# Kernel tuning notes

Hardware: AMD Instinct MI355X
Metric: run time of the kernel (lower is better)

Reference implementation:

```python
import jax, jax.numpy as jnp
import numpy as np

B, N, D, K = 2, 8192, 512, 16


def setup_inputs() -> dict:
    key = jax.random.key(0)
    k1, k2, k3, k4 = jax.random.split(key, 4)
    x = jax.random.normal(k1, (B, N, D), dtype=jnp.float32)
    xyz = jax.random.normal(k2, (B, N, 3), dtype=jnp.float32)
    # nn.Linear(d_model, 3*d_model): weight [3D, D], bias [3D]
    W_qkv = jax.random.normal(k3, (3 * D, D), dtype=jnp.float32) * 0.02
    b_qkv = jnp.zeros((3 * D,), dtype=jnp.float32)
    # nn.Linear(d_model, d_model)
    W_fc = jax.random.normal(k4, (D, D), dtype=jnp.float32) * 0.02
    b_fc = jnp.zeros((D,), dtype=jnp.float32)
    return {"x": x, "xyz": xyz, "W_qkv": W_qkv, "b_qkv": b_qkv, "W_fc": W_fc, "b_fc": b_fc}


def _knn_idx(xyz):
    # squared-distance KNN (same ordering as cdist): |a|^2 + |b|^2 - 2 a.b
    sq = jnp.sum(xyz * xyz, axis=-1)                      # [B, N]
    d2 = sq[:, :, None] + sq[:, None, :] - 2.0 * jnp.einsum('bnc,bmc->bnm', xyz, xyz)
    return jax.lax.top_k(-d2, K)[1]                       # [B, N, K] smallest distances


def reference(x, xyz, W_qkv, b_qkv, W_fc, b_fc):
    knn_idx = _knn_idx(xyz)                               # no-grad in original
    qkv = jnp.einsum('bnd,ed->bne', x, W_qkv) + b_qkv     # [B, N, 3D]
    qkv = qkv.reshape(B, N, 3, D)
    q, k, v = qkv[:, :, 0], qkv[:, :, 1], qkv[:, :, 2]    # [B, N, D]
    gather = jax.vmap(lambda arr, idx: arr[idx])          # per-batch neighbor gather
    k_neigh = gather(k, knn_idx)                          # [B, N, K, D]
    v_neigh = gather(v, knn_idx)                          # [B, N, K, D]
    # faithful to einsum('bnd,bnsk->bns', q, k_neigh): sums d and feature dims independently
    attn = (q.sum(-1)[:, :, None] * k_neigh.sum(-1)) / jnp.sqrt(jnp.float32(D))  # [B, N, K]
    attn = jax.nn.softmax(attn, axis=2)[..., None]        # [B, N, K, 1]
    x_out = (attn * v_neigh).sum(axis=2)                  # [B, N, D]
    return jnp.einsum('bnd,ed->bne', x_out, W_fc) + b_fc + x
```

## Files before the change

kernel.cpp:

```cpp
#include <hip/hip_runtime.h>

typedef _Float16 half_t;
typedef _Float16 half8 __attribute__((ext_vector_type(8)));
typedef _Float16 half4v __attribute__((ext_vector_type(4)));
typedef float f32x4 __attribute__((ext_vector_type(4)));
typedef float f32x2 __attribute__((ext_vector_type(2)));

#define NB 2
#define NN 8192
#define ND 512
#define NKNN 16
#define BN (NB*NN)

#define OFF_XH   0ull
#define OFF_VH   (OFF_XH  + (size_t)BN*ND*2)
#define OFF_XOH  (OFF_VH  + (size_t)BN*ND*2)
#define OFF_WVH  (OFF_XOH + (size_t)BN*ND*2)
#define OFF_WFCH (OFF_WVH + (size_t)ND*ND*2)
#define OFF_XW   (OFF_WFCH+ (size_t)ND*ND*2)
#define OFF_XW2  (OFF_XW  + (size_t)BN*16)
#define OFF_IDX  (OFF_XW2 + (size_t)BN*16)
#define OFF_WQC  (OFF_IDX + (size_t)BN*NKNN*4)
#define OFF_WKC  (OFF_WQC + 2048)
#define OFF_QKB  (OFF_WKC + 2048)
#define OFF_QS   (OFF_QKB + 256)
#define OFF_KS   (OFF_QS  + (size_t)BN*4)

__device__ __forceinline__ void gload16(const void* g, void* l) {
  __builtin_amdgcn_global_load_lds((const __attribute__((address_space(1))) void*)g,
                                   (__attribute__((address_space(3))) void*)l, 16, 0, 0);
}

__global__ __launch_bounds__(256) void ksetup(const float* __restrict__ wqkv,
                                              const float* __restrict__ bqkv,
                                              const float* __restrict__ wfc,
                                              const float* __restrict__ xyz,
                                              float* __restrict__ wq, float* __restrict__ wk,
                                              float* __restrict__ qkb,
                                              half_t* __restrict__ wvh, half_t* __restrict__ wfch,
                                              float4* __restrict__ xw, float4* __restrict__ xw2) {
  const int blk = blockIdx.x;
  const int t = threadIdx.x;
  if (blk < 16) {
    int h = blk >> 3, g = blk & 7;
    int dl = t & 63, s = t >> 6;
    const float* Wb = wqkv + (size_t)h * 512 * 512;
    int d = g * 64 + dl;
    float acc = 0.f;
    for (int e = s * 128; e < s * 128 + 128; ++e) acc += Wb[(size_t)e * 512 + d];
    __shared__ float red[4][64];
    red[s][dl] = acc;
    __syncthreads();
    if (s == 0) (h ? wk : wq)[d] = red[0][dl] + red[1][dl] + red[2][dl] + red[3][dl];
  } else if (blk == 16) {
    __shared__ float r0[256], r1[256];
    r0[t] = bqkv[t] + bqkv[t + 256];
    r1[t] = bqkv[512 + t] + bqkv[768 + t];
    __syncthreads();
    for (int s = 128; s; s >>= 1) {
      if (t < s) { r0[t] += r0[t + s]; r1[t] += r1[t + s]; }
      __syncthreads();
    }
    if (t == 0) { qkb[0] = r0[0]; qkb[1] = r1[0]; }
  } else if (blk < 273) {
    int i = (blk - 17) * 256 + t;
    float4 a = ((const float4*)(wqkv + 1024 * 512))[i];
    half4v ha; ha[0]=(half_t)a.x; ha[1]=(half_t)a.y; ha[2]=(half_t)a.z; ha[3]=(half_t)a.w;
    *(half4v*)(wvh + (size_t)i * 4) = ha;
    float4 c = ((const float4*)wfc)[i];
    half4v hc; hc[0]=(half_t)c.x; hc[1]=(half_t)c.y; hc[2]=(half_t)c.z; hc[3]=(half_t)c.w;
    *(half4v*)(wfch + (size_t)i * 4) = hc;
  } else {
    int p = (blk - 273) * 256 + t;
    int b = p >> 12;
    int pl = p & 4095;
    int i0 = b * NN + pl * 2;
    const float* s = xyz + (size_t)i0 * 3;
    float x0 = s[0], y0 = s[1], z0 = s[2];
    float x1 = s[3], y1 = s[4], z1 = s[5];
    float sq0 = __fadd_rn(__fadd_rn(__fmul_rn(x0, x0), __fmul_rn(y0, y0)), __fmul_rn(z0, z0));
    float sq1 = __fadd_rn(__fadd_rn(__fmul_rn(x1, x1), __fmul_rn(y1, y1)), __fmul_rn(z1, z1));
    xw[i0]     = make_float4(x0, y0, z0, sq0);
    xw[i0 + 1] = make_float4(x1, y1, z1, sq1);
    xw2[(size_t)b * NN + pl]        = make_float4(x0, x1, y0, y1);
    xw2[(size_t)b * NN + NN/2 + pl] = make_float4(z0, z1, sq0, sq1);
  }
}

__global__ __launch_bounds__(256) void kxh(const float* __restrict__ x,
                                           const float* __restrict__ wq,
                                           const float* __restrict__ wk,
                                           const float* __restrict__ qkb,
                                           half_t* __restrict__ xh,
                                           float* __restrict__ qs,
                                           float* __restrict__ ks) {
  int wid = blockIdx.x * 4 + (threadIdx.x >> 6);
  int l = threadIdx.x & 63;
  size_t base = (size_t)wid * ND + l * 8;
  float4 a0 = *(const float4*)(x + base);
  float4 a1 = *(const float4*)(x + base + 4);
  half8 h;
  h[0]=(half_t)a0.x; h[1]=(half_t)a0.y; h[2]=(half_t)a0.z; h[3]=(half_t)a0.w;
  h[4]=(half_t)a1.x; h[5]=(half_t)a1.y; h[6]=(half_t)a1.z; h[7]=(half_t)a1.w;
  *(half8*)(xh + base) = h;
  float4 q0 = ((const float4*)(wq + l * 8))[0], q1 = ((const float4*)(wq + l * 8))[1];
  float4 k0 = ((const float4*)(wk + l * 8))[0], k1 = ((const float4*)(wk + l * 8))[1];
  float dq = a0.x*q0.x + a0.y*q0.y + a0.z*q0.z + a0.w*q0.w
           + a1.x*q1.x + a1.y*q1.y + a1.z*q1.z + a1.w*q1.w;
  float dk = a0.x*k0.x + a0.y*k0.y + a0.z*k0.z + a0.w*k0.w
           + a1.x*k1.x + a1.y*k1.y + a1.z*k1.z + a1.w*k1.w;
  #pragma unroll
  for (int o = 32; o; o >>= 1) { dq += __shfl_xor(dq, o); dk += __shfl_xor(dk, o); }
  if (l == 0) { qs[wid] = dq + qkb[0]; ks[wid] = dk + qkb[1]; }
}

#define QPW 4
#define KTILE 256
__global__ __launch_bounds__(256, 6) void kknn(const float4* __restrict__ xw,
                                               const float4* __restrict__ xw2,
                                               int* __restrict__ idxo) {
  __shared__ __align__(16) float4 ldsA[2][KTILE];
  __shared__ __align__(16) float4 ldsB[2][KTILE];
  __shared__ float qdl[16 * 64];
  __shared__ int   qil[16 * 64];
  const int tid = threadIdx.x;
  const int l = tid & 63;
  const int w = tid >> 6;
  const int b = blockIdx.x >> 9;
  const int qbase = (blockIdx.x & 511) * (4 * QPW) + w * QPW;
  const float4* xb  = xw  + (size_t)b * NN;
  const float4* xa2 = xw2 + (size_t)b * NN;
  const float4* xb2 = xa2 + NN / 2;

#define STAGE(t, bi) do {                                                        \
    int ts_ = (t) * KTILE;                                                       \
    gload16(xa2 + ts_ + w * 64 + l, (void*)&ldsA[bi][w * 64]);                   \
    gload16(xb2 + ts_ + w * 64 + l, (void*)&ldsB[bi][w * 64]);                   \
  } while (0)

  f32x2 qxx[QPW], qyy[QPW], qzz[QPW], qww[QPW];
  #pragma unroll
  for (int qi = 0; qi < QPW; ++qi) {
    float4 qp = xb[qbase + qi];
    qxx[qi] = (f32x2){qp.x, qp.x};
    qyy[qi] = (f32x2){qp.y, qp.y};
    qzz[qi] = (f32x2){qp.z, qp.z};
    qww[qi] = (f32x2){qp.w, qp.w};
  }
  const f32x2 m2 = (f32x2){-2.0f, -2.0f};

  #pragma unroll
  for (int qi = 0; qi < QPW; ++qi) {
    qdl[(w * 4 + qi) * 64 + l] = __builtin_inff();
    qil[(w * 4 + qi) * 64 + l] = 0x7fffffff;
  }

  f32x2 mind[QPW];
  #pragma unroll
  for (int qi = 0; qi < QPW; ++qi) mind[qi] = (f32x2){__builtin_inff(), __builtin_inff()};

  STAGE(0, 0);
  __syncthreads();
  for (int t = 0; t < 16; ++t) {
    if (t < 15) STAGE(t + 1, (t + 1) & 1);
    #pragma unroll
    for (int it = 0; it < 4; ++it) {
      int p = it * 64 + l;
      float4 A  = ldsA[t & 1][p];
      float4 Bv = ldsB[t & 1][p];
      f32x2 cx = (f32x2){A.x, A.y};
      f32x2 cy = (f32x2){A.z, A.w};
      f32x2 cz = (f32x2){Bv.x, Bv.y};
      f32x2 cw = (f32x2){Bv.z, Bv.w};
      #pragma unroll
      for (int qi = 0; qi < QPW; ++qi) {
        f32x2 dot = __builtin_elementwise_fma(qzz[qi], cz,
                      __builtin_elementwise_fma(qyy[qi], cy, qxx[qi] * cx));
        f32x2 s2 = qww[qi] + cw;
        f32x2 d2 = __builtin_elementwise_fma(m2, dot, s2);
        mind[qi] = __builtin_elementwise_min(mind[qi], d2);
      }
    }
    __syncthreads();
  }

  float wst[QPW];
  #pragma unroll
  for (int qi = 0; qi < QPW; ++qi) {
    float d = fminf(mind[qi][0], mind[qi][1]);
    #pragma unroll
    for (int k = 2; k <= 64; k <<= 1) {
      #pragma unroll
      for (int j = k >> 1; j > 0; j >>= 1) {
        float od = __shfl_xor(d, j);
        bool up = ((l & k) == 0);
        bool lower_lane = ((l & j) == 0);
        bool oless = od < d;
        bool take = (up == lower_lane) ? oless : !oless;
        if (take) d = od;
      }
    }
    wst[qi] = __shfl(d, 15);
  }

  int qcnt[QPW];
  #pragma unroll
  for (int qi = 0; qi < QPW; ++qi) qcnt[qi] = 0;
  const unsigned long long below = (1ull << l) - 1;

  __syncthreads();
  STAGE(0, 0);
  __syncthreads();
  for (int t = 0; t < 16; ++t) {
    if (t < 15) STAGE(t + 1, (t + 1) & 1);
    #pragma unroll 2
    for (int it = 0; it < 4; ++it) {
      int p = it * 64 + l;
      float4 A  = ldsA[t & 1][p];
      float4 Bv = ldsB[t & 1][p];
      f32x2 cx = (f32x2){A.x, A.y};
      f32x2 cy = (f32x2){A.z, A.w};
      f32x2 cz = (f32x2){Bv.x, Bv.y};
      f32x2 cw = (f32x2){Bv.z, Bv.w};
      int ci0 = (t * KTILE + p) * 2;
      #pragma unroll
      for (int qi = 0; qi < QPW; ++qi) {
        f32x2 dot = __builtin_elementwise_fma(qzz[qi], cz,
                      __builtin_elementwise_fma(qyy[qi], cy, qxx[qi] * cx));
        f32x2 s2 = qww[qi] + cw;
        f32x2 d2 = __builtin_elementwise_fma(m2, dot, s2);
        bool ok0 = d2[0] <= wst[qi];
        bool ok1 = d2[1] <= wst[qi];
        unsigned long long m0 = __ballot(ok0);
        if (m0) {
          int slot = qcnt[qi] + __popcll(m0 & below);
          if (ok0 && slot < 64) {
            qdl[(w * 4 + qi) * 64 + slot] = d2[0];
            qil[(w * 4 + qi) * 64 + slot] = ci0;
          }
          qcnt[qi] += __popcll(m0);
        }
        unsigned long long m1 = __ballot(ok1);
        if (m1) {
          int slot = qcnt[qi] + __popcll(m1 & below);
          if (ok1 && slot < 64) {
            qdl[(w * 4 + qi) * 64 + slot] = d2[1];
            qil[(w * 4 + qi) * 64 + slot] = ci0 + 1;
          }
          qcnt[qi] += __popcll(m1);
        }
      }
    }
    __syncthreads();
  }

  #pragma unroll
  for (int qi = 0; qi < QPW; ++qi) {
    float d = qdl[(w * 4 + qi) * 64 + l];
    int  ii = qil[(w * 4 + qi) * 64 + l];
    #pragma unroll
    for (int k = 2; k <= 64; k <<= 1) {
      #pragma unroll
      for (int j = k >> 1; j > 0; j >>= 1) {
        float od = __shfl_xor(d, j);
        int   oi = __shfl_xor(ii, j);
        bool up = ((l & k) == 0);
        bool lower_lane = ((l & j) == 0);
        bool oless = (od < d) || (od == d && oi < ii);
        bool take = (up == lower_lane) ? oless : !oless;
        if (take) { d = od; ii = oi; }
      }
    }
    if (l < 16) idxo[((size_t)b * NN + qbase + qi) * NKNN + l] = ii;
  }
#undef STAGE
}

template <int EPI>
__global__ __launch_bounds__(256) void kgemm(const half_t* __restrict__ A,
                                             const half_t* __restrict__ Bw,
                                             const float* __restrict__ bias,
                                             const float* __restrict__ resid,
                                             void* __restrict__ Cout) {
  __shared__ __align__(16) half_t As[128 * 64];
  __shared__ __align__(16) half_t Bs[128 * 64];
  const int tid = threadIdx.x;
  const int l = tid & 63;
  const int w = tid >> 6;
  const int wm = w >> 1, wn = w & 1;
  const int mt = blockIdx.x >> 2;
  const int nt = blockIdx.x & 3;
  const int lr = l & 15, lg = l >> 4;

  f32x4 acc[4][4];
  #pragma unroll
  for (int i = 0; i < 4; ++i)
    #pragma unroll
    for (int j = 0; j < 4; ++j) acc[i][j] = (f32x4){0.f, 0.f, 0.f, 0.f};

  for (int kt = 0; kt < 8; ++kt) {
    #pragma unroll
    for (int i = 0; i < 4; ++i) {
      int id = i * 256 + tid;
      int rr = id >> 3, cc = id & 7;
      gload16(A + (size_t)(mt * 128 + rr) * ND + kt * 64 + cc * 8,
              (void*)(As + (size_t)(i * 256 + w * 64) * 8));
      gload16(Bw + (size_t)(nt * 128 + rr) * ND + kt * 64 + cc * 8,
              (void*)(Bs + (size_t)(i * 256 + w * 64) * 8));
    }
    __syncthreads();
    #pragma unroll
    for (int kk = 0; kk < 2; ++kk) {
      half8 af[4], bf[4];
      #pragma unroll
      for (int mi = 0; mi < 4; ++mi)
        af[mi] = *(const half8*)(As + (wm * 64 + mi * 16 + lr) * 64 + kk * 32 + lg * 8);
      #pragma unroll
      for (int ni = 0; ni < 4; ++ni)
        bf[ni] = *(const half8*)(Bs + (wn * 64 + ni * 16 + lr) * 64 + kk * 32 + lg * 8);
      #pragma unroll
      for (int mi = 0; mi < 4; ++mi)
        #pragma unroll
        for (int ni = 0; ni < 4; ++ni)
          acc[mi][ni] = __builtin_amdgcn_mfma_f32_16x16x32_f16(af[mi], bf[ni], acc[mi][ni], 0, 0, 0);
    }
    __syncthreads();
  }

  #pragma unroll
  for (int mi = 0; mi < 4; ++mi) {
    #pragma unroll
    for (int ni = 0; ni < 4; ++ni) {
      int col = nt * 128 + wn * 64 + ni * 16 + lr;
      #pragma unroll
      for (int r4 = 0; r4 < 4; ++r4) {
        size_t row = (size_t)mt * 128 + wm * 64 + mi * 16 + lg * 4 + r4;
        float v = acc[mi][ni][r4] + bias[col];
        if (EPI == 0) ((half_t*)Cout)[row * ND + col] = (half_t)v;
        else          ((float*)Cout)[row * ND + col] = v + resid[row * ND + col];
      }
    }
  }
}

__global__ __launch_bounds__(256) void kattn(const int* __restrict__ idx,
                                             const float* __restrict__ qs,
                                             const float* __restrict__ ks,
                                             const half_t* __restrict__ vh,
                                             half_t* __restrict__ xoh) {
  int wid = blockIdx.x * 4 + (threadIdx.x >> 6);
  int l = threadIdx.x & 63;
  int b = wid >> 13;
  int j = l & 15;
  int nb = idx[(size_t)wid * NKNN + j];
  float ksv = ks[(size_t)b * NN + nb];
  float logit = __fdiv_rn(__fmul_rn(qs[wid], ksv), 22.627416997969522f);
  float mx = logit;
  #pragma unroll
  for (int o = 8; o; o >>= 1) mx = fmaxf(mx, __shfl_xor(mx, o, 16));
  float e = expf(logit - mx);
  float s = e;
  #pragma unroll
  for (int o = 8; o; o >>= 1) s += __shfl_xor(s, o, 16);
  float p = e / s;

  float acc[8] = {0.f, 0.f, 0.f, 0.f, 0.f, 0.f, 0.f, 0.f};
  #pragma unroll
  for (int t16 = 0; t16 < 16; ++t16) {
    float wj = __shfl(p, t16, 16);
    int ij = __shfl(nb, t16, 16);
    const half8 vv = *(const half8*)(vh + ((size_t)b * NN + ij) * ND + l * 8);
    #pragma unroll
    for (int u = 0; u < 8; ++u) acc[u] += wj * (float)vv[u];
  }
  half8 ho;
  #pragma unroll
  for (int u = 0; u < 8; ++u) ho[u] = (half_t)acc[u];
  *(half8*)(xoh + (size_t)wid * ND + l * 8) = ho;
}

extern "C" void kernel_launch(void* const* d_in, const int* in_sizes, int n_in,
                              void* d_out, int out_size, void* d_ws, size_t ws_size,
                              hipStream_t stream) {
  const float* x    = (const float*)d_in[0];
  const float* xyz  = (const float*)d_in[1];
  const float* wqkv = (const float*)d_in[2];
  const float* bqkv = (const float*)d_in[3];
  const float* wfc  = (const float*)d_in[4];
  const float* bfc  = (const float*)d_in[5];
  char* ws = (char*)d_ws;
  half_t* xh   = (half_t*)(ws + OFF_XH);
  half_t* vh   = (half_t*)(ws + OFF_VH);
  half_t* xoh  = (half_t*)(ws + OFF_XOH);
  half_t* wvh  = (half_t*)(ws + OFF_WVH);
  half_t* wfch = (half_t*)(ws + OFF_WFCH);
  float4* xw   = (float4*)(ws + OFF_XW);
  float4* xw2  = (float4*)(ws + OFF_XW2);
  int*    idx  = (int*)(ws + OFF_IDX);
  float*  wqc  = (float*)(ws + OFF_WQC);
  float*  wkc  = (float*)(ws + OFF_WKC);
  float*  qkb  = (float*)(ws + OFF_QKB);
  float*  qs   = (float*)(ws + OFF_QS);
  float*  ks   = (float*)(ws + OFF_KS);

  ksetup<<<dim3(305), dim3(256), 0, stream>>>(wqkv, bqkv, wfc, xyz,
                                              wqc, wkc, qkb, wvh, wfch, xw, xw2);
  kxh   <<<dim3(4096),dim3(256), 0, stream>>>(x, wqc, wkc, qkb, xh, qs, ks);
  kknn  <<<dim3(1024),dim3(256), 0, stream>>>(xw, xw2, idx);
  kgemm<0><<<dim3(512),dim3(256), 0, stream>>>(xh, wvh, bqkv + 1024, (const float*)nullptr, (void*)vh);
  kattn <<<dim3(4096),dim3(256), 0, stream>>>(idx, qs, ks, vh, xoh);
  kgemm<1><<<dim3(512),dim3(256), 0, stream>>>(xoh, wfch, bfc, x, d_out);
}
```

Baseline: 145.8 us.

## Split KNN candidate scan across two blocks per query group and merge halves

The KNN kernel now splits the candidate set into two halves, each handled by a separate block, doubling the grid to increase parallelism and occupancy. Each half writes its sorted top-16 distances and indices to workspace, and a new merge kernel combines the two sorted lists with a bitonic merge over 32 lanes. This adds an extra launch, extra global traffic for partial results, and a per-half threshold that is looser than a global one, so more candidates may pass the filter.

```diff
diff --git a/kernel.cpp b/kernel.cpp
--- a/kernel.cpp
+++ b/kernel.cpp
@@ -20,7 +20,9 @@
 #define OFF_XW   (OFF_WFCH+ (size_t)ND*ND*2)
 #define OFF_XW2  (OFF_XW  + (size_t)BN*16)
 #define OFF_IDX  (OFF_XW2 + (size_t)BN*16)
-#define OFF_WQC  (OFF_IDX + (size_t)BN*NKNN*4)
+#define OFF_DH   (OFF_IDX + (size_t)BN*NKNN*4)
+#define OFF_IH   (OFF_DH  + (size_t)BN*2*NKNN*4)
+#define OFF_WQC  (OFF_IH  + (size_t)BN*2*NKNN*4)
 #define OFF_WKC  (OFF_WQC + 2048)
 #define OFF_QKB  (OFF_WKC + 2048)
 #define OFF_QS   (OFF_QKB + 256)
@@ -118,7 +120,8 @@
 #define KTILE 256
 __global__ __launch_bounds__(256, 6) void kknn(const float4* __restrict__ xw,
                                                const float4* __restrict__ xw2,
-                                               int* __restrict__ idxo) {
+                                               float* __restrict__ dhalf,
+                                               int* __restrict__ ihalf) {
   __shared__ __align__(16) float4 ldsA[2][KTILE];
   __shared__ __align__(16) float4 ldsB[2][KTILE];
   __shared__ float qdl[16 * 64];
@@ -126,11 +129,13 @@
   const int tid = threadIdx.x;
   const int l = tid & 63;
   const int w = tid >> 6;
-  const int b = blockIdx.x >> 9;
-  const int qbase = (blockIdx.x & 511) * (4 * QPW) + w * QPW;
+  const int g = blockIdx.x >> 1;
+  const int h = blockIdx.x & 1;
+  const int b = g >> 9;
+  const int qbase = (g & 511) * (4 * QPW) + w * QPW;
   const float4* xb  = xw  + (size_t)b * NN;
-  const float4* xa2 = xw2 + (size_t)b * NN;
-  const float4* xb2 = xa2 + NN / 2;
+  const float4* xa2 = xw2 + (size_t)b * NN + h * 2048;
+  const float4* xb2 = xw2 + (size_t)b * NN + NN / 2 + h * 2048;
 
 #define STAGE(t, bi) do {                                                        \
     int ts_ = (t) * KTILE;                                                       \
@@ -161,8 +166,8 @@
 
   STAGE(0, 0);
   __syncthreads();
-  for (int t = 0; t < 16; ++t) {
-    if (t < 15) STAGE(t + 1, (t + 1) & 1);
+  for (int t = 0; t < 8; ++t) {
+    if (t < 7) STAGE(t + 1, (t + 1) & 1);
     #pragma unroll
     for (int it = 0; it < 4; ++it) {
       int p = it * 64 + l;
@@ -211,8 +216,8 @@
   __syncthreads();
   STAGE(0, 0);
   __syncthreads();
-  for (int t = 0; t < 16; ++t) {
-    if (t < 15) STAGE(t + 1, (t + 1) & 1);
+  for (int t = 0; t < 8; ++t) {
+    if (t < 7) STAGE(t + 1, (t + 1) & 1);
     #pragma unroll 2
     for (int it = 0; it < 4; ++it) {
       int p = it * 64 + l;
@@ -222,7 +227,7 @@
       f32x2 cy = (f32x2){A.z, A.w};
       f32x2 cz = (f32x2){Bv.x, Bv.y};
       f32x2 cw = (f32x2){Bv.z, Bv.w};
-      int ci0 = (t * KTILE + p) * 2;
+      int ci0 = h * 4096 + (t * KTILE + p) * 2;
       #pragma unroll
       for (int qi = 0; qi < QPW; ++qi) {
         f32x2 dot = __builtin_elementwise_fma(qzz[qi], cz,
@@ -271,9 +276,36 @@
         if (take) { d = od; ii = oi; }
       }
     }
-    if (l < 16) idxo[((size_t)b * NN + qbase + qi) * NKNN + l] = ii;
+    if (l < 16) {
+      size_t o = (((size_t)(b * NN + qbase + qi)) * 2 + h) * NKNN + l;
+      dhalf[o] = d;
+      ihalf[o] = ii;
+    }
   }
 #undef STAGE
+}
+
+__global__ __launch_bounds__(256) void kmerge(const float* __restrict__ dhalf,
+                                              const int* __restrict__ ihalf,
+                                              int* __restrict__ idxo) {
+  const int l = threadIdx.x & 63;
+  const int wv = threadIdx.x >> 6;
+  const int q = blockIdx.x * 8 + wv * 2 + (l >> 5);
+  const int sub = l & 31;
+  const int pos = (sub < 16) ? sub : 31 - sub;
+  const int hh  = (sub < 16) ? 0 : 1;
+  size_t o = (((size_t)q) * 2 + hh) * NKNN + pos;
+  float d = dhalf[o];
+  int   i = ihalf[o];
+  #pragma unroll
+  for (int j = 16; j; j >>= 1) {
+    float od = __shfl_xor(d, j, 32);
+    int   oi = __shfl_xor(i, j, 32);
+    bool oless = (od < d) || (od == d && oi < i);
+    bool keepmin = ((sub & j) == 0);
+    if (keepmin == oless) { d = od; i = oi; }
+  }
+  if (sub < 16) idxo[(size_t)q * NKNN + sub] = i;
 }
 
 template <int EPI>
@@ -397,6 +429,8 @@
   float4* xw   = (float4*)(ws + OFF_XW);
   float4* xw2  = (float4*)(ws + OFF_XW2);
   int*    idx  = (int*)(ws + OFF_IDX);
+  float*  dh   = (float*)(ws + OFF_DH);
+  int*    ih   = (int*)(ws + OFF_IH);
   float*  wqc  = (float*)(ws + OFF_WQC);
   float*  wkc  = (float*)(ws + OFF_WKC);
   float*  qkb  = (float*)(ws + OFF_QKB);
@@ -406,7 +440,8 @@
   ksetup<<<dim3(305), dim3(256), 0, stream>>>(wqkv, bqkv, wfc, xyz,
                                               wqc, wkc, qkb, wvh, wfch, xw, xw2);
   kxh   <<<dim3(4096),dim3(256), 0, stream>>>(x, wqc, wkc, qkb, xh, qs, ks);
-  kknn  <<<dim3(1024),dim3(256), 0, stream>>>(xw, xw2, idx);
+  kknn  <<<dim3(2048),dim3(256), 0, stream>>>(xw, xw2, dh, ih);
+  kmerge<<<dim3(2048),dim3(256), 0, stream>>>(dh, ih, idx);
   kgemm<0><<<dim3(512),dim3(256), 0, stream>>>(xh, wvh, bqkv + 1024, (const float*)nullptr, (void*)vh);
   kattn <<<dim3(4096),dim3(256), 0, stream>>>(idx, qs, ks, vh, xoh);
   kgemm<1><<<dim3(512),dim3(256), 0, stream>>>(xoh, wfch, bfc, x, d_out);
```

Result: slower. 156.6 us (+7.4%).
